# Performance work log

Hardware: AMD Instinct MI355X
Metric: run time of the kernel (lower is better)

## Reference

```python
import jax, jax.numpy as jnp
import numpy as np

N_HEADS = 16
HEAD_DIM = 128

def _apply_rope(x, cos, sin):
    # x: [B, H, T, D]; cos/sin: [T, D//2]
    B, H, T, D = x.shape
    xp = x.astype(jnp.float32).reshape(B, H, T, D // 2, 2)
    x0, x1 = xp[..., 0], xp[..., 1]
    c = cos[None, None, :T, :]
    s = sin[None, None, :T, :]
    # complex multiply (x0 + i x1) * (c + i s)
    r0 = x0 * c - x1 * s
    r1 = x0 * s + x1 * c
    out = jnp.stack([r0, r1], axis=-1).reshape(B, H, T, D)
    return out.astype(x.dtype)

def setup_inputs() -> dict:
    key = jax.random.key(0)
    ks = jax.random.split(key, 7)
    B, T, C = 2, 2048, 2048
    Dh = C // N_HEADS
    sc = 1.0 / np.sqrt(C)
    x = jax.random.normal(ks[0], (B, T, C), dtype=jnp.float32)
    # rotary frequencies like precompute_freqs_cis
    pos = jnp.arange(T, dtype=jnp.float32)
    inv = 1.0 / (10000.0 ** (jnp.arange(0, Dh, 2, dtype=jnp.float32) / Dh))
    ang = pos[:, None] * inv[None, :]  # [T, Dh//2]
    freqs_cos = jnp.cos(ang)
    freqs_sin = jnp.sin(ang)
    wq = jax.random.normal(ks[1], (C, C), dtype=jnp.float32) * sc
    wk = jax.random.normal(ks[2], (C, C), dtype=jnp.float32) * sc
    wv = jax.random.normal(ks[3], (C, C), dtype=jnp.float32) * sc
    wo = jax.random.normal(ks[4], (C, C), dtype=jnp.float32) * sc
    return {"x": x, "freqs_cos": freqs_cos, "freqs_sin": freqs_sin,
            "wq": wq, "wk": wk, "wv": wv, "wo": wo}

def reference(x, freqs_cos, freqs_sin, wq, wk, wv, wo):
    B, T, C = x.shape
    H, D = N_HEADS, HEAD_DIM
    # nn.Linear applies x @ W.T
    q = (x @ wq.T).reshape(B, T, H, D).transpose(0, 2, 1, 3)
    k = (x @ wk.T).reshape(B, T, H, D).transpose(0, 2, 1, 3)
    v = (x @ wv.T).reshape(B, T, H, D).transpose(0, 2, 1, 3)
    q = _apply_rope(q, freqs_cos, freqs_sin)
    k = _apply_rope(k, freqs_cos, freqs_sin)
    scale = 1.0 / np.sqrt(D)
    attn = jnp.einsum('bhqd,bhkd->bhqk', q, k) * scale  # [B,H,T,T]
    causal = jnp.tril(jnp.ones((T, T), dtype=bool))
    attn = jnp.where(causal[None, None], attn, -jnp.inf)
    attn = jax.nn.softmax(attn, axis=-1)
    out = jnp.einsum('bhqk,bhkd->bhqd', attn, v)
    out = out.transpose(0, 2, 1, 3).reshape(B, T, C)
    return out @ wo.T
```

## Files before the change

kernel.cpp:

```cpp
#include <hip/hip_runtime.h>
#include <hip/hip_bf16.h>
#include <stdint.h>


typedef short bf16x8 __attribute__((ext_vector_type(8)));
typedef float f32x4  __attribute__((ext_vector_type(4)));

static __device__ __forceinline__ short f2bf(float f) {
  unsigned u = __builtin_bit_cast(unsigned, f);
  u = (u + 0x7fffu + ((u >> 16) & 1u)) >> 16;
  return (short)u;
}
static __device__ __forceinline__ float bf2f(short s) {
  unsigned u = ((unsigned)(unsigned short)s) << 16;
  return __builtin_bit_cast(float, u);
}
static __device__ __forceinline__ void gload_lds16(const void* g, void* l) {
  auto gp = (const __attribute__((address_space(1))) void*)(g);
  auto lp = (__attribute__((address_space(3))) void*)(l);
  __builtin_amdgcn_global_load_lds(gp, lp, 16, 0, 0);
}

__global__ __launch_bounds__(256) void cast8_kernel(const float* __restrict__ in,
                                                    short* __restrict__ out, int n8) {
  int g = blockIdx.x * 256 + threadIdx.x;
  if (g >= n8) return;
  const float4* p = (const float4*)(in + (size_t)g * 8);
  float4 a = p[0], b = p[1];
  bf16x8 o;
  o[0] = f2bf(a.x); o[1] = f2bf(a.y); o[2] = f2bf(a.z); o[3] = f2bf(a.w);
  o[4] = f2bf(b.x); o[5] = f2bf(b.y); o[6] = f2bf(b.z); o[7] = f2bf(b.w);
  *(bf16x8*)(out + (size_t)g * 8) = o;
}

__global__ __launch_bounds__(256) void castw_kernel(const float* __restrict__ w0,
                                                    const float* __restrict__ w1,
                                                    const float* __restrict__ w2,
                                                    const float* __restrict__ w3,
                                                    short* __restrict__ out) {
  int seg = blockIdx.y;
  const float* in = (seg == 0) ? w0 : (seg == 1) ? w1 : (seg == 2) ? w2 : w3;
  short* o = out + (size_t)seg * 4194304;
  int g = blockIdx.x * 256 + threadIdx.x;
  const float4* p = (const float4*)(in + (size_t)g * 8);
  float4 a = p[0], b = p[1];
  bf16x8 v;
  v[0] = f2bf(a.x); v[1] = f2bf(a.y); v[2] = f2bf(a.z); v[3] = f2bf(a.w);
  v[4] = f2bf(b.x); v[5] = f2bf(b.y); v[6] = f2bf(b.z); v[7] = f2bf(b.w);
  *(bf16x8*)(o + (size_t)g * 8) = v;
}

__global__ __launch_bounds__(256) void rope_kernel(short* __restrict__ qk,
                                                   const float* __restrict__ cs,
                                                   const float* __restrict__ sn,
                                                   float scale) {
  int g = blockIdx.x * 256 + threadIdx.x;
  size_t e0 = (size_t)g * 8;
  int d0 = (int)(e0 & 127);
  int t  = (int)((e0 >> 7) & 2047);
  bf16x8 v = *(bf16x8*)(qk + e0);
  float4 c = *(const float4*)(cs + t * 64 + (d0 >> 1));
  float4 s = *(const float4*)(sn + t * 64 + (d0 >> 1));
  float cc[4] = {c.x, c.y, c.z, c.w};
  float ss[4] = {s.x, s.y, s.z, s.w};
  bf16x8 o;
#pragma unroll
  for (int i = 0; i < 4; ++i) {
    float x0 = bf2f(v[2 * i]), x1 = bf2f(v[2 * i + 1]);
    o[2 * i]     = f2bf((x0 * cc[i] - x1 * ss[i]) * scale);
    o[2 * i + 1] = f2bf((x0 * ss[i] + x1 * cc[i]) * scale);
  }
  *(bf16x8*)(qk + e0) = o;
}

__global__ __launch_bounds__(256) void transpose_v(const short* __restrict__ vb,
                                                   short* __restrict__ vt) {
  __shared__ char L[8192] __attribute__((aligned(128)));
  int bx = blockIdx.x;
  int bh = bx >> 6, rest = bx & 63, tt = rest >> 1, td = rest & 1;
  int t0 = tt * 64, d0 = td * 64;
  size_t base = (size_t)bh * (2048 * 128);
#pragma unroll
  for (int it = 0; it < 2; ++it) {
    int c = it * 256 + threadIdx.x;
    int t = c >> 3, dc = c & 7;
    bf16x8 v = *(const bf16x8*)(vb + base + (size_t)(t0 + t) * 128 + d0 + dc * 8);
#pragma unroll
    for (int i = 0; i < 8; ++i) {
      int d = dc * 8 + i;
      int g = (d & 7) ^ ((d >> 3) & 7);
      *(short*)(L + d * 128 + (((t >> 3) ^ g) * 16) + (t & 7) * 2) = v[i];
    }
  }
  __syncthreads();
#pragma unroll
  for (int it = 0; it < 2; ++it) {
    int c = it * 256 + threadIdx.x;
    int dr = c >> 3, tc = c & 7;
    int g = (dr & 7) ^ ((dr >> 3) & 7);
    bf16x8 v = *(const bf16x8*)(L + dr * 128 + ((tc ^ g) * 16));
    *(bf16x8*)(vt + base + (size_t)(d0 + dr) * 2048 + t0 + tc * 8) = v;
  }
}

template <int MODE>
__global__ __launch_bounds__(256) void gemm_bt(const short* __restrict__ A,
                                               const short* __restrict__ W0,
                                               const short* __restrict__ W1,
                                               const short* __restrict__ W2,
                                               short* __restrict__ oq,
                                               short* __restrict__ ok_,
                                               short* __restrict__ ov,
                                               float* __restrict__ of, int NT) {
  __shared__ char lds[16384] __attribute__((aligned(128)));
  int nwg = gridDim.x;
  int bid = blockIdx.x;
  int wg = (bid & 7) * (nwg >> 3) + (bid >> 3);
  int mt = wg / NT, nt = wg % NT;
  const int lane = threadIdx.x & 63;
  const int wid = threadIdx.x >> 6;
  const int wr = wid >> 1, wc = wid & 1;
  const int l15 = lane & 15, l4 = lane >> 4;
  const short* Wp;
  int n0, wsel = 0;
  if (MODE == 0) {
    wsel = nt >> 4;
    Wp = (wsel == 0) ? W0 : ((wsel == 1) ? W1 : W2);
    n0 = (nt & 15) * 128;
  } else {
    Wp = W0;
    n0 = nt * 128;
  }
  const int m0 = mt * 128;
  const f32x4 vzero = {0.f, 0.f, 0.f, 0.f};
  f32x4 acc[4][4];
#pragma unroll
  for (int i = 0; i < 4; ++i)
#pragma unroll
    for (int j = 0; j < 4; ++j) acc[i][j] = vzero;
  const short* Ab = A + (size_t)m0 * 2048;
  const short* Wb = Wp + (size_t)n0 * 2048;
  for (int k0 = 0; k0 < 2048; k0 += 32) {
#pragma unroll
    for (int j = 0; j < 2; ++j) {
      int c = j * 256 + (int)threadIdx.x;
      int row = c >> 2, slot = c & 3;
      int ldsoff = (c - lane) * 16;
      gload_lds16(Ab + (size_t)row * 2048 + k0 + slot * 8, lds + ldsoff);
      gload_lds16(Wb + (size_t)row * 2048 + k0 + slot * 8, lds + 8192 + ldsoff);
    }
    __syncthreads();
    bf16x8 af[4], wf[4];
#pragma unroll
    for (int i = 0; i < 4; ++i) {
      af[i] = *(const bf16x8*)(lds + (wr * 64 + i * 16 + l15) * 64 + l4 * 16);
      wf[i] = *(const bf16x8*)(lds + 8192 + (wc * 64 + i * 16 + l15) * 64 + l4 * 16);
    }
#pragma unroll
    for (int i = 0; i < 4; ++i)
#pragma unroll
      for (int j = 0; j < 4; ++j)
        acc[i][j] = __builtin_amdgcn_mfma_f32_16x16x32_bf16(af[i], wf[j], acc[i][j], 0, 0, 0);
    __syncthreads();
  }
#pragma unroll
  for (int mi = 0; mi < 4; ++mi) {
#pragma unroll
    for (int j = 0; j < 4; ++j) {
      int rr = m0 + wr * 64 + mi * 16 + l4 * 4 + j;
#pragma unroll
      for (int ni = 0; ni < 4; ++ni) {
        int cc = n0 + wc * 64 + ni * 16 + l15;
        float v = acc[mi][ni][j];
        if (MODE == 0) {
          int b = rr >> 11, t = rr & 2047, h = cc >> 7, d = cc & 127;
          short* o = (wsel == 0) ? oq : ((wsel == 1) ? ok_ : ov);
          o[(((size_t)b * 16 + h) * 2048 + t) * 128 + d] = f2bf(v);
        } else {
          of[(size_t)rr * 2048 + cc] = v;
        }
      }
    }
  }
}

__global__ __launch_bounds__(256) void attn_kernel(const short* __restrict__ qb,
                                                   const short* __restrict__ kb,
                                                   const short* __restrict__ vt,
                                                   short* __restrict__ aout) {
  __shared__ char lds[40960] __attribute__((aligned(128)));
  const int lane = threadIdx.x & 63;
  const int w = threadIdx.x >> 6;
  const int l15 = lane & 15, l4 = lane >> 4;
  int bid0 = blockIdx.x;
  int bid = (bid0 & 7) * 64 + (bid0 >> 3);
  const int bh = bid >> 4, p = bid & 15;
  const size_t qkbase = (size_t)bh * (2048 * 128);
  char* Pb = lds + 32768 + w * 2048;
  const f32x4 vzero = {0.f, 0.f, 0.f, 0.f};

#pragma unroll 1
  for (int half = 0; half < 2; ++half) {
    const int qtile = half ? (31 - p) : p;
    const int qbase = qtile << 6;
    const int qrow = qbase + w * 16 + l15;
    bf16x8 aq[4];
#pragma unroll
    for (int ks = 0; ks < 4; ++ks)
      aq[ks] = *(const bf16x8*)(qb + qkbase + (size_t)qrow * 128 + ks * 32 + l4 * 8);
    f32x4 accO[8];
#pragma unroll
    for (int nt = 0; nt < 8; ++nt) accO[nt] = vzero;
    float m_[4], l_[4];
#pragma unroll
    for (int j = 0; j < 4; ++j) { m_[j] = -1e30f; l_[j] = 0.f; }

#pragma unroll 1
    for (int kt = 0; kt <= qtile; ++kt) {
#pragma unroll
      for (int j = 0; j < 4; ++j) {
        int c = j * 256 + (int)threadIdx.x;
        int ldsoff = (c - lane) * 16;
        {
          int row = c >> 4, slot = c & 15;
          gload_lds16(kb + qkbase + (size_t)(kt * 64 + row) * 128 + ((slot ^ (row & 7)) * 8),
                      lds + ldsoff);
        }
        {
          int row = c >> 3, slot = c & 7;
          gload_lds16(vt + qkbase + (size_t)row * 2048 + kt * 64 + ((slot ^ (row & 7)) * 8),
                      lds + 16384 + ldsoff);
        }
      }
      __syncthreads();

      f32x4 s[4];
#pragma unroll
      for (int ct = 0; ct < 4; ++ct) {
        s[ct] = vzero;
        int kcol = ct * 16 + l15;
#pragma unroll
        for (int ks = 0; ks < 4; ++ks) {
          bf16x8 bk = *(const bf16x8*)(lds + kcol * 256 + ((ks * 64 + l4 * 16) ^ ((kcol & 7) << 4)));
          s[ct] = __builtin_amdgcn_mfma_f32_16x16x32_bf16(aq[ks], bk, s[ct], 0, 0, 0);
        }
      }
      if (kt * 64 + 63 > qbase + w * 16) {
#pragma unroll
        for (int ct = 0; ct < 4; ++ct) {
          int kc = kt * 64 + ct * 16 + l15;
#pragma unroll
          for (int j = 0; j < 4; ++j) {
            int r = qbase + w * 16 + l4 * 4 + j;
            if (kc > r) s[ct][j] = -1e30f;
          }
        }
      }
#pragma unroll
      for (int j = 0; j < 4; ++j) {
        float mx = fmaxf(fmaxf(s[0][j], s[1][j]), fmaxf(s[2][j], s[3][j]));
        mx = fmaxf(mx, __shfl_xor(mx, 1));
        mx = fmaxf(mx, __shfl_xor(mx, 2));
        mx = fmaxf(mx, __shfl_xor(mx, 4));
        mx = fmaxf(mx, __shfl_xor(mx, 8));
        float mn = fmaxf(m_[j], mx);
        float resc = __expf(m_[j] - mn);
        m_[j] = mn;
        float rs = 0.f;
#pragma unroll
        for (int ct = 0; ct < 4; ++ct) {
          float e = __expf(s[ct][j] - mn);
          s[ct][j] = e;
          rs += e;
        }
        rs += __shfl_xor(rs, 1);
        rs += __shfl_xor(rs, 2);
        rs += __shfl_xor(rs, 4);
        rs += __shfl_xor(rs, 8);
        l_[j] = l_[j] * resc + rs;
#pragma unroll
        for (int nt = 0; nt < 8; ++nt) accO[nt][j] *= resc;
      }
#pragma unroll
      for (int ct = 0; ct < 4; ++ct)
#pragma unroll
        for (int j = 0; j < 4; ++j) {
          int r = l4 * 4 + j, cc = ct * 16 + l15;
          *(short*)(Pb + r * 128 + ((cc * 2) ^ ((r & 7) << 4))) = f2bf(s[ct][j]);
        }
      __threadfence_block();
#pragma unroll
      for (int ks2 = 0; ks2 < 2; ++ks2) {
        bf16x8 pa = *(const bf16x8*)(Pb + l15 * 128 + ((ks2 * 64 + l4 * 16) ^ ((l15 & 7) << 4)));
#pragma unroll
        for (int nt = 0; nt < 8; ++nt) {
          int d = nt * 16 + l15;
          bf16x8 bv = *(const bf16x8*)(lds + 16384 + d * 128 + ((ks2 * 64 + l4 * 16) ^ ((d & 7) << 4)));
          accO[nt] = __builtin_amdgcn_mfma_f32_16x16x32_bf16(pa, bv, accO[nt], 0, 0, 0);
        }
      }
      __syncthreads();
    }
    const int b = bh >> 4, h = bh & 15;
#pragma unroll
    for (int j = 0; j < 4; ++j) {
      float inv = 1.0f / l_[j];
      int t = qbase + w * 16 + l4 * 4 + j;
      size_t obase = ((size_t)(b * 2048 + t)) * 2048 + h * 128;
#pragma unroll
      for (int nt = 0; nt < 8; ++nt)
        aout[obase + nt * 16 + l15] = f2bf(accO[nt][j] * inv);
    }
  }
}

extern "C" void kernel_launch(void* const* d_in, const int* in_sizes, int n_in,
                              void* d_out, int out_size, void* d_ws, size_t ws_size,
                              hipStream_t stream) {
  const float* x  = (const float*)d_in[0];
  const float* fc = (const float*)d_in[1];
  const float* fs = (const float*)d_in[2];
  const float* wq = (const float*)d_in[3];
  const float* wk = (const float*)d_in[4];
  const float* wv = (const float*)d_in[5];
  const float* wo = (const float*)d_in[6];

  short* ws  = (short*)d_ws;
  short* xb  = ws;
  short* wqb = ws + 8388608;
  short* wkb = ws + 12582912;
  short* wvb = ws + 16777216;
  short* wob = ws + 20971520;
  short* qb  = ws + 25165824;
  short* kb  = ws + 33554432;
  short* vb  = ws + 41943040;
  short* vt  = xb;
  short* aout = vb;

  cast8_kernel<<<4096, 256, 0, stream>>>(x, xb, 1048576);
  castw_kernel<<<dim3(2048, 4), 256, 0, stream>>>(wq, wk, wv, wo, wqb);
  gemm_bt<0><<<1536, 256, 0, stream>>>(xb, wqb, wkb, wvb, qb, kb, vb, nullptr, 48);
  rope_kernel<<<4096, 256, 0, stream>>>(qb, fc, fs, 0.08838834764831845f);
  rope_kernel<<<4096, 256, 0, stream>>>(kb, fc, fs, 1.0f);
  transpose_v<<<2048, 256, 0, stream>>>(vb, vt);
  attn_kernel<<<512, 256, 0, stream>>>(qb, kb, vt, aout);
  gemm_bt<1><<<512, 256, 0, stream>>>(aout, wob, nullptr, nullptr,
                                      nullptr, nullptr, nullptr, (float*)d_out, 16);
}
```

Measured before the change: 420.8 us.

## Pipeline GEMMs with triple-buffered LDS, fuse RoPE into QKV epilogue, double-buffer attention

The GEMM kernel now runs 512 threads on a 128x256 tile with a K step of 64. It keeps three LDS stages, swizzles their layout, and waits with explicit vmcnt so global loads overlap the MFMA work. RoPE and the Q scaling move into the QKV GEMM epilogue using lane shuffles, which removes two elementwise kernel launches and their extra passes over memory. The attention kernel double-buffers its K/V tiles and raises wave priority around the MFMA blocks. The cost is that the GEMM uses about 144KB of LDS at one block per CU, which lowers occupancy, and the reworked grid is smaller.

```diff
diff --git a/kernel.cpp b/kernel.cpp
--- a/kernel.cpp
+++ b/kernel.cpp
@@ -20,6 +20,7 @@
   auto lp = (__attribute__((address_space(3))) void*)(l);
   __builtin_amdgcn_global_load_lds(gp, lp, 16, 0, 0);
 }
+#define VMCNT(n) asm volatile("s_waitcnt vmcnt(" #n ")" ::: "memory")
 
 __global__ __launch_bounds__(256) void cast8_kernel(const float* __restrict__ in,
                                                     short* __restrict__ out, int n8) {
@@ -50,29 +51,6 @@
   *(bf16x8*)(o + (size_t)g * 8) = v;
 }
 
-__global__ __launch_bounds__(256) void rope_kernel(short* __restrict__ qk,
-                                                   const float* __restrict__ cs,
-                                                   const float* __restrict__ sn,
-                                                   float scale) {
-  int g = blockIdx.x * 256 + threadIdx.x;
-  size_t e0 = (size_t)g * 8;
-  int d0 = (int)(e0 & 127);
-  int t  = (int)((e0 >> 7) & 2047);
-  bf16x8 v = *(bf16x8*)(qk + e0);
-  float4 c = *(const float4*)(cs + t * 64 + (d0 >> 1));
-  float4 s = *(const float4*)(sn + t * 64 + (d0 >> 1));
-  float cc[4] = {c.x, c.y, c.z, c.w};
-  float ss[4] = {s.x, s.y, s.z, s.w};
-  bf16x8 o;
-#pragma unroll
-  for (int i = 0; i < 4; ++i) {
-    float x0 = bf2f(v[2 * i]), x1 = bf2f(v[2 * i + 1]);
-    o[2 * i]     = f2bf((x0 * cc[i] - x1 * ss[i]) * scale);
-    o[2 * i + 1] = f2bf((x0 * ss[i] + x1 * cc[i]) * scale);
-  }
-  *(bf16x8*)(qk + e0) = o;
-}
-
 __global__ __launch_bounds__(256) void transpose_v(const short* __restrict__ vb,
                                                    short* __restrict__ vt) {
   __shared__ char L[8192] __attribute__((aligned(128)));
@@ -104,83 +82,140 @@
 }
 
 template <int MODE>
-__global__ __launch_bounds__(256) void gemm_bt(const short* __restrict__ A,
-                                               const short* __restrict__ W0,
-                                               const short* __restrict__ W1,
-                                               const short* __restrict__ W2,
-                                               short* __restrict__ oq,
-                                               short* __restrict__ ok_,
-                                               short* __restrict__ ov,
-                                               float* __restrict__ of, int NT) {
-  __shared__ char lds[16384] __attribute__((aligned(128)));
+__global__ __launch_bounds__(512, 1) void gemm8(const short* __restrict__ A,
+                                                const short* __restrict__ W0,
+                                                const short* __restrict__ W1,
+                                                const short* __restrict__ W2,
+                                                short* __restrict__ oq,
+                                                short* __restrict__ ok_,
+                                                short* __restrict__ ov,
+                                                float* __restrict__ of,
+                                                const float* __restrict__ fc,
+                                                const float* __restrict__ fs,
+                                                int NT) {
+  const int SB = 49152;
+  __shared__ char lds[147456] __attribute__((aligned(128)));
   int nwg = gridDim.x;
   int bid = blockIdx.x;
   int wg = (bid & 7) * (nwg >> 3) + (bid >> 3);
   int mt = wg / NT, nt = wg % NT;
-  const int lane = threadIdx.x & 63;
-  const int wid = threadIdx.x >> 6;
-  const int wr = wid >> 1, wc = wid & 1;
+  const int tid = threadIdx.x;
+  const int lane = tid & 63;
+  const int wid = tid >> 6;
+  const int wr = wid >> 2, wc = wid & 3;
   const int l15 = lane & 15, l4 = lane >> 4;
   const short* Wp;
   int n0, wsel = 0;
   if (MODE == 0) {
-    wsel = nt >> 4;
+    wsel = nt >> 3;
     Wp = (wsel == 0) ? W0 : ((wsel == 1) ? W1 : W2);
-    n0 = (nt & 15) * 128;
+    n0 = (nt & 7) * 256;
   } else {
     Wp = W0;
-    n0 = nt * 128;
+    n0 = nt * 256;
   }
   const int m0 = mt * 128;
+  const short* Ab = A + (size_t)m0 * 2048;
+  const short* Wb = Wp + (size_t)n0 * 2048;
+
   const f32x4 vzero = {0.f, 0.f, 0.f, 0.f};
   f32x4 acc[4][4];
 #pragma unroll
   for (int i = 0; i < 4; ++i)
 #pragma unroll
     for (int j = 0; j < 4; ++j) acc[i][j] = vzero;
-  const short* Ab = A + (size_t)m0 * 2048;
-  const short* Wb = Wp + (size_t)n0 * 2048;
-  for (int k0 = 0; k0 < 2048; k0 += 32) {
+
+  auto stage = [&](int b, int t) {
+    int k0 = t * 64;
+    char* La = lds + b * SB;
+    char* Lb = La + 16384;
 #pragma unroll
     for (int j = 0; j < 2; ++j) {
-      int c = j * 256 + (int)threadIdx.x;
-      int row = c >> 2, slot = c & 3;
-      int ldsoff = (c - lane) * 16;
-      gload_lds16(Ab + (size_t)row * 2048 + k0 + slot * 8, lds + ldsoff);
-      gload_lds16(Wb + (size_t)row * 2048 + k0 + slot * 8, lds + 8192 + ldsoff);
-    }
-    __syncthreads();
-    bf16x8 af[4], wf[4];
-#pragma unroll
-    for (int i = 0; i < 4; ++i) {
-      af[i] = *(const bf16x8*)(lds + (wr * 64 + i * 16 + l15) * 64 + l4 * 16);
-      wf[i] = *(const bf16x8*)(lds + 8192 + (wc * 64 + i * 16 + l15) * 64 + l4 * 16);
-    }
-#pragma unroll
-    for (int i = 0; i < 4; ++i)
-#pragma unroll
-      for (int j = 0; j < 4; ++j)
-        acc[i][j] = __builtin_amdgcn_mfma_f32_16x16x32_bf16(af[i], wf[j], acc[i][j], 0, 0, 0);
-    __syncthreads();
-  }
-#pragma unroll
-  for (int mi = 0; mi < 4; ++mi) {
+      int c = j * 512 + tid;
+      int row = c >> 3, slot = c & 7;
+      gload_lds16(Ab + (size_t)row * 2048 + k0 + ((slot ^ (row & 7)) * 8),
+                  La + (c - lane) * 16);
+    }
 #pragma unroll
     for (int j = 0; j < 4; ++j) {
-      int rr = m0 + wr * 64 + mi * 16 + l4 * 4 + j;
-#pragma unroll
-      for (int ni = 0; ni < 4; ++ni) {
-        int cc = n0 + wc * 64 + ni * 16 + l15;
-        float v = acc[mi][ni][j];
-        if (MODE == 0) {
-          int b = rr >> 11, t = rr & 2047, h = cc >> 7, d = cc & 127;
-          short* o = (wsel == 0) ? oq : ((wsel == 1) ? ok_ : ov);
+      int c = j * 512 + tid;
+      int row = c >> 3, slot = c & 7;
+      gload_lds16(Wb + (size_t)row * 2048 + k0 + ((slot ^ (row & 7)) * 8),
+                  Lb + (c - lane) * 16);
+    }
+  };
+
+  stage(0, 0);
+  stage(1, 1);
+  VMCNT(6);
+  __builtin_amdgcn_s_barrier();
+
+  int cb = 0, sb = 2;
+#pragma unroll 1
+  for (int t = 0; t < 32; ++t) {
+    if (t + 2 < 32) stage(sb, t + 2);
+    const char* La = lds + cb * SB;
+    const char* Lb = La + 16384;
+#pragma unroll
+    for (int kk = 0; kk < 2; ++kk) {
+      bf16x8 af[4], wf[4];
+#pragma unroll
+      for (int i = 0; i < 4; ++i) {
+        int Ra = wr * 64 + i * 16 + l15;
+        af[i] = *(const bf16x8*)(La + Ra * 128 + (((kk * 4 + l4) ^ (Ra & 7)) << 4));
+        int Rb = wc * 64 + i * 16 + l15;
+        wf[i] = *(const bf16x8*)(Lb + Rb * 128 + (((kk * 4 + l4) ^ (Rb & 7)) << 4));
+      }
+      __builtin_amdgcn_s_setprio(1);
+#pragma unroll
+      for (int mi = 0; mi < 4; ++mi)
+#pragma unroll
+        for (int ni = 0; ni < 4; ++ni)
+          acc[mi][ni] = __builtin_amdgcn_mfma_f32_16x16x32_bf16(af[mi], wf[ni], acc[mi][ni], 0, 0, 0);
+      __builtin_amdgcn_s_setprio(0);
+    }
+    if (t + 2 < 32) { VMCNT(6); } else { VMCNT(0); }
+    __builtin_amdgcn_s_barrier();
+    cb = (cb == 2) ? 0 : cb + 1;
+    sb = (sb == 2) ? 0 : sb + 1;
+  }
+
+  if (MODE == 0) {
+    short* o = (wsel == 0) ? oq : ((wsel == 1) ? ok_ : ov);
+#pragma unroll
+    for (int mi = 0; mi < 4; ++mi) {
+#pragma unroll
+      for (int j = 0; j < 4; ++j) {
+        int rr = m0 + wr * 64 + mi * 16 + l4 * 4 + j;
+        int b = rr >> 11, t = rr & 2047;
+#pragma unroll
+        for (int ni = 0; ni < 4; ++ni) {
+          int cc = n0 + wc * 64 + ni * 16 + l15;
+          int h = cc >> 7, d = cc & 127;
+          float v = acc[mi][ni][j];
+          if (wsel < 2) {
+            float vp = __shfl_xor(v, 1);
+            float c = fc[t * 64 + (d >> 1)];
+            float s = fs[t * 64 + (d >> 1)];
+            v = (lane & 1) ? (vp * s + v * c) : (v * c - vp * s);
+            if (wsel == 0) v *= 0.08838834764831845f;
+          }
           o[(((size_t)b * 16 + h) * 2048 + t) * 128 + d] = f2bf(v);
-        } else {
-          of[(size_t)rr * 2048 + cc] = v;
-        }
-      }
-    }
+        }
+      }
+    }
+  } else {
+#pragma unroll
+    for (int mi = 0; mi < 4; ++mi)
+#pragma unroll
+      for (int j = 0; j < 4; ++j) {
+        int rr = m0 + wr * 64 + mi * 16 + l4 * 4 + j;
+#pragma unroll
+        for (int ni = 0; ni < 4; ++ni) {
+          int cc = n0 + wc * 64 + ni * 16 + l15;
+          of[(size_t)rr * 2048 + cc] = acc[mi][ni][j];
+        }
+      }
   }
 }
 
@@ -188,16 +223,35 @@
                                                    const short* __restrict__ kb,
                                                    const short* __restrict__ vt,
                                                    short* __restrict__ aout) {
-  __shared__ char lds[40960] __attribute__((aligned(128)));
-  const int lane = threadIdx.x & 63;
-  const int w = threadIdx.x >> 6;
+  __shared__ char lds[73728] __attribute__((aligned(128)));
+  const int tid = threadIdx.x;
+  const int lane = tid & 63;
+  const int w = tid >> 6;
   const int l15 = lane & 15, l4 = lane >> 4;
   int bid0 = blockIdx.x;
   int bid = (bid0 & 7) * 64 + (bid0 >> 3);
   const int bh = bid >> 4, p = bid & 15;
   const size_t qkbase = (size_t)bh * (2048 * 128);
-  char* Pb = lds + 32768 + w * 2048;
+  char* Pb = lds + 65536 + w * 2048;
   const f32x4 vzero = {0.f, 0.f, 0.f, 0.f};
+
+  auto stage = [&](int b, int kt) {
+#pragma unroll
+    for (int j = 0; j < 4; ++j) {
+      int c = j * 256 + tid;
+      int ldsoff = (c - lane) * 16;
+      {
+        int row = c >> 4, slot = c & 15;
+        gload_lds16(kb + qkbase + (size_t)(kt * 64 + row) * 128 + ((slot ^ (row & 7)) * 8),
+                    lds + b * 32768 + ldsoff);
+      }
+      {
+        int row = c >> 3, slot = c & 7;
+        gload_lds16(vt + qkbase + (size_t)row * 2048 + kt * 64 + ((slot ^ (row & 7)) * 8),
+                    lds + b * 32768 + 16384 + ldsoff);
+      }
+    }
+  };
 
 #pragma unroll 1
   for (int half = 0; half < 2; ++half) {
@@ -215,36 +269,30 @@
 #pragma unroll
     for (int j = 0; j < 4; ++j) { m_[j] = -1e30f; l_[j] = 0.f; }
 
+    stage(0, 0);
+    VMCNT(0);
+    __builtin_amdgcn_s_barrier();
+
 #pragma unroll 1
     for (int kt = 0; kt <= qtile; ++kt) {
-#pragma unroll
-      for (int j = 0; j < 4; ++j) {
-        int c = j * 256 + (int)threadIdx.x;
-        int ldsoff = (c - lane) * 16;
-        {
-          int row = c >> 4, slot = c & 15;
-          gload_lds16(kb + qkbase + (size_t)(kt * 64 + row) * 128 + ((slot ^ (row & 7)) * 8),
-                      lds + ldsoff);
-        }
-        {
-          int row = c >> 3, slot = c & 7;
-          gload_lds16(vt + qkbase + (size_t)row * 2048 + kt * 64 + ((slot ^ (row & 7)) * 8),
-                      lds + 16384 + ldsoff);
-        }
-      }
-      __syncthreads();
+      const int cbuf = kt & 1;
+      if (kt < qtile) stage(cbuf ^ 1, kt + 1);
+      const char* Kl = lds + cbuf * 32768;
+      const char* Vl = Kl + 16384;
 
       f32x4 s[4];
+      __builtin_amdgcn_s_setprio(1);
 #pragma unroll
       for (int ct = 0; ct < 4; ++ct) {
         s[ct] = vzero;
         int kcol = ct * 16 + l15;
 #pragma unroll
         for (int ks = 0; ks < 4; ++ks) {
-          bf16x8 bk = *(const bf16x8*)(lds + kcol * 256 + ((ks * 64 + l4 * 16) ^ ((kcol & 7) << 4)));
+          bf16x8 bk = *(const bf16x8*)(Kl + kcol * 256 + ((ks * 64 + l4 * 16) ^ ((kcol & 7) << 4)));
           s[ct] = __builtin_amdgcn_mfma_f32_16x16x32_bf16(aq[ks], bk, s[ct], 0, 0, 0);
         }
       }
+      __builtin_amdgcn_s_setprio(0);
       if (kt * 64 + 63 > qbase + w * 16) {
 #pragma unroll
         for (int ct = 0; ct < 4; ++ct) {
@@ -289,17 +337,20 @@
           *(short*)(Pb + r * 128 + ((cc * 2) ^ ((r & 7) << 4))) = f2bf(s[ct][j]);
         }
       __threadfence_block();
+      __builtin_amdgcn_s_setprio(1);
 #pragma unroll
       for (int ks2 = 0; ks2 < 2; ++ks2) {
         bf16x8 pa = *(const bf16x8*)(Pb + l15 * 128 + ((ks2 * 64 + l4 * 16) ^ ((l15 & 7) << 4)));
 #pragma unroll
         for (int nt = 0; nt < 8; ++nt) {
           int d = nt * 16 + l15;
-          bf16x8 bv = *(const bf16x8*)(lds + 16384 + d * 128 + ((ks2 * 64 + l4 * 16) ^ ((d & 7) << 4)));
+          bf16x8 bv = *(const bf16x8*)(Vl + d * 128 + ((ks2 * 64 + l4 * 16) ^ ((d & 7) << 4)));
           accO[nt] = __builtin_amdgcn_mfma_f32_16x16x32_bf16(pa, bv, accO[nt], 0, 0, 0);
         }
       }
-      __syncthreads();
+      __builtin_amdgcn_s_setprio(0);
+      VMCNT(0);
+      __builtin_amdgcn_s_barrier();
     }
     const int b = bh >> 4, h = bh & 15;
 #pragma unroll
@@ -339,11 +390,10 @@
 
   cast8_kernel<<<4096, 256, 0, stream>>>(x, xb, 1048576);
   castw_kernel<<<dim3(2048, 4), 256, 0, stream>>>(wq, wk, wv, wo, wqb);
-  gemm_bt<0><<<1536, 256, 0, stream>>>(xb, wqb, wkb, wvb, qb, kb, vb, nullptr, 48);
-  rope_kernel<<<4096, 256, 0, stream>>>(qb, fc, fs, 0.08838834764831845f);
-  rope_kernel<<<4096, 256, 0, stream>>>(kb, fc, fs, 1.0f);
+  gemm8<0><<<768, 512, 0, stream>>>(xb, wqb, wkb, wvb, qb, kb, vb, nullptr, fc, fs, 24);
   transpose_v<<<2048, 256, 0, stream>>>(vb, vt);
   attn_kernel<<<512, 256, 0, stream>>>(qb, kb, vt, aout);
-  gemm_bt<1><<<512, 256, 0, stream>>>(aout, wob, nullptr, nullptr,
-                                      nullptr, nullptr, nullptr, (float*)d_out, 16);
-}
+  gemm8<1><<<256, 512, 0, stream>>>(aout, wob, nullptr, nullptr,
+                                    nullptr, nullptr, nullptr, (float*)d_out,
+                                    nullptr, nullptr, 8);
+}
```

Result: no change. 422.1 us (+0.3%).

## Double-buffer K tiles, read V from global, lazy softmax rescale, one q-tile per block

Applied to the files above, without the earlier changes.

Restructures the attention kernel so each block handles a single q-tile (1024 blocks, longest tiles scheduled first) instead of a paired causal half. K tiles are double-buffered in LDS with async global-to-LDS loads that overlap compute, and V fragments are read straight from global memory instead of through LDS. The online softmax skips the rescale of the running max and accumulator unless the max grows by more than a threshold, and P is converted to bf16 with a cheaper rounding. It also adds s_setprio around the MFMA sections. The costs are less even load balance per block, uncoalesced and uncached V reads from global, and slightly different numerics from the deferred rescale and fast rounding.

```diff
diff --git a/kernel.cpp b/kernel.cpp
--- a/kernel.cpp
+++ b/kernel.cpp
@@ -11,6 +11,10 @@
   u = (u + 0x7fffu + ((u >> 16) & 1u)) >> 16;
   return (short)u;
 }
+static __device__ __forceinline__ short f2bf_fast(float f) {
+  unsigned u = __builtin_bit_cast(unsigned, f);
+  return (short)((u + 0x8000u) >> 16);
+}
 static __device__ __forceinline__ float bf2f(short s) {
   unsigned u = ((unsigned)(unsigned short)s) << 16;
   return __builtin_bit_cast(float, u);
@@ -20,6 +24,7 @@
   auto lp = (__attribute__((address_space(3))) void*)(l);
   __builtin_amdgcn_global_load_lds(gp, lp, 16, 0, 0);
 }
+#define VMCNT(n) asm volatile("s_waitcnt vmcnt(" #n ")" ::: "memory")
 
 __global__ __launch_bounds__(256) void cast8_kernel(const float* __restrict__ in,
                                                     short* __restrict__ out, int n8) {
@@ -189,81 +194,91 @@
                                                    const short* __restrict__ vt,
                                                    short* __restrict__ aout) {
   __shared__ char lds[40960] __attribute__((aligned(128)));
-  const int lane = threadIdx.x & 63;
-  const int w = threadIdx.x >> 6;
+  const int tid = threadIdx.x;
+  const int lane = tid & 63;
+  const int w = tid >> 6;
   const int l15 = lane & 15, l4 = lane >> 4;
-  int bid0 = blockIdx.x;
-  int bid = (bid0 & 7) * 64 + (bid0 >> 3);
-  const int bh = bid >> 4, p = bid & 15;
-  const size_t qkbase = (size_t)bh * (2048 * 128);
+  const int bid0 = blockIdx.x;
+  const int xcd = bid0 & 7, idx = bid0 >> 3;
+  const int bh = xcd * 4 + (idx & 3);
+  const int qt = 31 - (idx >> 2);
+  const size_t base = (size_t)bh * (2048 * 128);
   char* Pb = lds + 32768 + w * 2048;
   const f32x4 vzero = {0.f, 0.f, 0.f, 0.f};
+  const int qbase = qt << 6;
+
+  auto stage = [&](int b, int kt) {
+#pragma unroll
+    for (int j = 0; j < 4; ++j) {
+      int c = j * 256 + tid;
+      int row = c >> 4, slot = c & 15;
+      gload_lds16(kb + base + (size_t)(kt * 64 + row) * 128 + ((slot ^ (row & 7)) * 8),
+                  lds + b * 16384 + (c - lane) * 16);
+    }
+  };
+
+  const int qrow = qbase + w * 16 + l15;
+  bf16x8 aq[4];
+#pragma unroll
+  for (int ks = 0; ks < 4; ++ks)
+    aq[ks] = *(const bf16x8*)(qb + base + (size_t)qrow * 128 + ks * 32 + l4 * 8);
+  f32x4 accO[8];
+#pragma unroll
+  for (int nt = 0; nt < 8; ++nt) accO[nt] = vzero;
+  float m_[4], l_[4];
+#pragma unroll
+  for (int j = 0; j < 4; ++j) { m_[j] = -1e30f; l_[j] = 0.f; }
+
+  stage(0, 0);
+  VMCNT(0);
+  __builtin_amdgcn_s_barrier();
 
 #pragma unroll 1
-  for (int half = 0; half < 2; ++half) {
-    const int qtile = half ? (31 - p) : p;
-    const int qbase = qtile << 6;
-    const int qrow = qbase + w * 16 + l15;
-    bf16x8 aq[4];
-#pragma unroll
-    for (int ks = 0; ks < 4; ++ks)
-      aq[ks] = *(const bf16x8*)(qb + qkbase + (size_t)qrow * 128 + ks * 32 + l4 * 8);
-    f32x4 accO[8];
-#pragma unroll
-    for (int nt = 0; nt < 8; ++nt) accO[nt] = vzero;
-    float m_[4], l_[4];
-#pragma unroll
-    for (int j = 0; j < 4; ++j) { m_[j] = -1e30f; l_[j] = 0.f; }
-
-#pragma unroll 1
-    for (int kt = 0; kt <= qtile; ++kt) {
+  for (int kt = 0; kt <= qt; ++kt) {
+    const int cbuf = kt & 1;
+    if (kt < qt) stage(cbuf ^ 1, kt + 1);
+    const char* Kl = lds + cbuf * 16384;
+
+    f32x4 s[4];
+    __builtin_amdgcn_s_setprio(1);
+#pragma unroll
+    for (int ct = 0; ct < 4; ++ct) {
+      s[ct] = vzero;
+      int kcol = ct * 16 + l15;
+#pragma unroll
+      for (int ks = 0; ks < 4; ++ks) {
+        bf16x8 bk = *(const bf16x8*)(Kl + kcol * 256 + ((ks * 64 + l4 * 16) ^ ((kcol & 7) << 4)));
+        s[ct] = __builtin_amdgcn_mfma_f32_16x16x32_bf16(aq[ks], bk, s[ct], 0, 0, 0);
+      }
+    }
+    __builtin_amdgcn_s_setprio(0);
+    if (kt == qt) {
+#pragma unroll
+      for (int ct = 0; ct < 4; ++ct) {
+        int kc = kt * 64 + ct * 16 + l15;
+#pragma unroll
+        for (int j = 0; j < 4; ++j) {
+          int r = qbase + w * 16 + l4 * 4 + j;
+          if (kc > r) s[ct][j] = -1e30f;
+        }
+      }
+    }
+    float mx4[4];
+    float need = 0.f;
+#pragma unroll
+    for (int j = 0; j < 4; ++j) {
+      float mx = fmaxf(fmaxf(s[0][j], s[1][j]), fmaxf(s[2][j], s[3][j]));
+      mx = fmaxf(mx, __shfl_xor(mx, 1));
+      mx = fmaxf(mx, __shfl_xor(mx, 2));
+      mx = fmaxf(mx, __shfl_xor(mx, 4));
+      mx = fmaxf(mx, __shfl_xor(mx, 8));
+      mx4[j] = mx;
+      need = fmaxf(need, mx - m_[j]);
+    }
+    if (__any(need > 4.0f)) {
 #pragma unroll
       for (int j = 0; j < 4; ++j) {
-        int c = j * 256 + (int)threadIdx.x;
-        int ldsoff = (c - lane) * 16;
-        {
-          int row = c >> 4, slot = c & 15;
-          gload_lds16(kb + qkbase + (size_t)(kt * 64 + row) * 128 + ((slot ^ (row & 7)) * 8),
-                      lds + ldsoff);
-        }
-        {
-          int row = c >> 3, slot = c & 7;
-          gload_lds16(vt + qkbase + (size_t)row * 2048 + kt * 64 + ((slot ^ (row & 7)) * 8),
-                      lds + 16384 + ldsoff);
-        }
-      }
-      __syncthreads();
-
-      f32x4 s[4];
-#pragma unroll
-      for (int ct = 0; ct < 4; ++ct) {
-        s[ct] = vzero;
-        int kcol = ct * 16 + l15;
-#pragma unroll
-        for (int ks = 0; ks < 4; ++ks) {
-          bf16x8 bk = *(const bf16x8*)(lds + kcol * 256 + ((ks * 64 + l4 * 16) ^ ((kcol & 7) << 4)));
-          s[ct] = __builtin_amdgcn_mfma_f32_16x16x32_bf16(aq[ks], bk, s[ct], 0, 0, 0);
-        }
-      }
-      if (kt * 64 + 63 > qbase + w * 16) {
-#pragma unroll
-        for (int ct = 0; ct < 4; ++ct) {
-          int kc = kt * 64 + ct * 16 + l15;
-#pragma unroll
-          for (int j = 0; j < 4; ++j) {
-            int r = qbase + w * 16 + l4 * 4 + j;
-            if (kc > r) s[ct][j] = -1e30f;
-          }
-        }
-      }
-#pragma unroll
-      for (int j = 0; j < 4; ++j) {
-        float mx = fmaxf(fmaxf(s[0][j], s[1][j]), fmaxf(s[2][j], s[3][j]));
-        mx = fmaxf(mx, __shfl_xor(mx, 1));
-        mx = fmaxf(mx, __shfl_xor(mx, 2));
-        mx = fmaxf(mx, __shfl_xor(mx, 4));
-        mx = fmaxf(mx, __shfl_xor(mx, 8));
-        float mn = fmaxf(m_[j], mx);
+        float mn = fmaxf(m_[j], mx4[j]);
         float resc = __expf(m_[j] - mn);
         m_[j] = mn;
         float rs = 0.f;
@@ -281,36 +296,55 @@
 #pragma unroll
         for (int nt = 0; nt < 8; ++nt) accO[nt][j] *= resc;
       }
-#pragma unroll
-      for (int ct = 0; ct < 4; ++ct)
-#pragma unroll
-        for (int j = 0; j < 4; ++j) {
-          int r = l4 * 4 + j, cc = ct * 16 + l15;
-          *(short*)(Pb + r * 128 + ((cc * 2) ^ ((r & 7) << 4))) = f2bf(s[ct][j]);
+    } else {
+#pragma unroll
+      for (int j = 0; j < 4; ++j) {
+        float rs = 0.f;
+#pragma unroll
+        for (int ct = 0; ct < 4; ++ct) {
+          float e = __expf(s[ct][j] - m_[j]);
+          s[ct][j] = e;
+          rs += e;
         }
-      __threadfence_block();
-#pragma unroll
-      for (int ks2 = 0; ks2 < 2; ++ks2) {
-        bf16x8 pa = *(const bf16x8*)(Pb + l15 * 128 + ((ks2 * 64 + l4 * 16) ^ ((l15 & 7) << 4)));
-#pragma unroll
-        for (int nt = 0; nt < 8; ++nt) {
-          int d = nt * 16 + l15;
-          bf16x8 bv = *(const bf16x8*)(lds + 16384 + d * 128 + ((ks2 * 64 + l4 * 16) ^ ((d & 7) << 4)));
-          accO[nt] = __builtin_amdgcn_mfma_f32_16x16x32_bf16(pa, bv, accO[nt], 0, 0, 0);
-        }
-      }
-      __syncthreads();
-    }
-    const int b = bh >> 4, h = bh & 15;
-#pragma unroll
-    for (int j = 0; j < 4; ++j) {
-      float inv = 1.0f / l_[j];
-      int t = qbase + w * 16 + l4 * 4 + j;
-      size_t obase = ((size_t)(b * 2048 + t)) * 2048 + h * 128;
-#pragma unroll
-      for (int nt = 0; nt < 8; ++nt)
-        aout[obase + nt * 16 + l15] = f2bf(accO[nt][j] * inv);
-    }
+        rs += __shfl_xor(rs, 1);
+        rs += __shfl_xor(rs, 2);
+        rs += __shfl_xor(rs, 4);
+        rs += __shfl_xor(rs, 8);
+        l_[j] += rs;
+      }
+    }
+#pragma unroll
+    for (int ct = 0; ct < 4; ++ct)
+#pragma unroll
+      for (int j = 0; j < 4; ++j) {
+        int r = l4 * 4 + j, cc = ct * 16 + l15;
+        *(short*)(Pb + r * 128 + ((cc * 2) ^ ((r & 7) << 4))) = f2bf_fast(s[ct][j]);
+      }
+    __threadfence_block();
+    __builtin_amdgcn_s_setprio(1);
+#pragma unroll
+    for (int ks2 = 0; ks2 < 2; ++ks2) {
+      bf16x8 pa = *(const bf16x8*)(Pb + l15 * 128 + ((ks2 * 64 + l4 * 16) ^ ((l15 & 7) << 4)));
+#pragma unroll
+      for (int nt = 0; nt < 8; ++nt) {
+        int d = nt * 16 + l15;
+        bf16x8 bv = *(const bf16x8*)(vt + base + (size_t)d * 2048 + kt * 64 + ks2 * 32 + l4 * 8);
+        accO[nt] = __builtin_amdgcn_mfma_f32_16x16x32_bf16(pa, bv, accO[nt], 0, 0, 0);
+      }
+    }
+    __builtin_amdgcn_s_setprio(0);
+    VMCNT(0);
+    __builtin_amdgcn_s_barrier();
+  }
+  const int b = bh >> 4, h = bh & 15;
+#pragma unroll
+  for (int j = 0; j < 4; ++j) {
+    float inv = 1.0f / l_[j];
+    int t = qbase + w * 16 + l4 * 4 + j;
+    size_t obase = ((size_t)(b * 2048 + t)) * 2048 + h * 128;
+#pragma unroll
+    for (int nt = 0; nt < 8; ++nt)
+      aout[obase + nt * 16 + l15] = f2bf(accO[nt][j] * inv);
   }
 }
 
@@ -343,7 +377,7 @@
   rope_kernel<<<4096, 256, 0, stream>>>(qb, fc, fs, 0.08838834764831845f);
   rope_kernel<<<4096, 256, 0, stream>>>(kb, fc, fs, 1.0f);
   transpose_v<<<2048, 256, 0, stream>>>(vb, vt);
-  attn_kernel<<<512, 256, 0, stream>>>(qb, kb, vt, aout);
+  attn_kernel<<<1024, 256, 0, stream>>>(qb, kb, vt, aout);
   gemm_bt<1><<<512, 256, 0, stream>>>(aout, wob, nullptr, nullptr,
                                       nullptr, nullptr, nullptr, (float*)d_out, 16);
 }
```

Measured after the change: 507.7 us. 1.21x slower.
